# Kernel optimization log

Measured on AMD Instinct MI355X. Metric: run time of the kernel, lower is better.

Reference implementation:

```python
import jax, jax.numpy as jnp
import numpy as np

B, QUE, VAL, D = 4, 128, 128, 512

def setup_inputs() -> dict:
    key = jax.random.key(0)
    k = jax.random.split(key, 8)
    return {
        "qs_1": jax.random.normal(k[0], (B, QUE, D), jnp.float32),
        "qs_2": jax.random.normal(k[1], (B, QUE, D), jnp.float32),  # unused by forward, kept for signature fidelity
        "ks":   jax.random.normal(k[2], (B, VAL, D), jnp.float32),
        "vs":   jax.random.normal(k[3], (B, VAL, D), jnp.float32),
        "sg_mask": jax.random.randint(k[4], (B, VAL), 0, 2).astype(bool),  # True = masked
        "W1":  jax.random.normal(k[5], (D, D), jnp.float32) / np.sqrt(D),
        "b1":  jnp.zeros((D,), jnp.float32),
        "Wse": jax.random.normal(k[6], (D, D), jnp.float32) / np.sqrt(D),
        "bse": jnp.zeros((D,), jnp.float32),
        "W2":  jax.random.normal(k[7], (D, 1), jnp.float32) / np.sqrt(D),
        "b2":  jnp.zeros((1,), jnp.float32),
    }

def reference(qs_1, qs_2, ks, vs, sg_mask, W1, b1, Wse, bse, W2, b2):
    # Pairwise query-key elementwise product: [B, que, val, d]
    x = qs_1[:, :, None, :] * ks[:, None, :, :]
    # linear1: Linear(d,d) + ReLU (dropout = identity at eval)
    h = jax.nn.relu(jnp.einsum('bqvd,de->bqve', x, W1) + b1)
    # linear2: Linear(d,1) + ReLU -> scalar score per (q, v) pair
    s = jax.nn.relu(jnp.einsum('bqvd,do->bqvo', h, W2) + b2)[..., 0]  # [B, que, val]
    m = sg_mask[:, None, :]                      # [B, 1, val], True = masked out
    # masked mean of h over the val axis (masked_fill(0) then divide by valid count)
    h = jnp.where(m[..., None], 0.0, h)
    denom = jnp.sum(~sg_mask, axis=-1).astype(h.dtype)      # [B]
    mean = h.sum(axis=2) / denom[:, None, None]             # [B, que, d]
    # squeeze-excitation gate: sigmoid(relu(Linear(d,d)))
    gate = jax.nn.sigmoid(jax.nn.relu(mean @ Wse + bse))    # [B, que, d]
    # masked softmax over val, weighted sum of values
    s = jnp.where(m, -1e9, s)
    w = jax.nn.softmax(s, axis=-1)                          # [B, que, val]
    out = jnp.einsum('bqv,bvd->bqd', w, vs)                 # [B, que, d]
    return gate * out
```

## Files before the change

### kernel.cpp

```cpp
#include <hip/hip_runtime.h>
#include <stdint.h>
#include <stddef.h>

#define BDIM 4
#define QUE  128
#define VAL  128
#define DD   512
#define BQ   (BDIM*QUE)
#define BK   64

typedef float    f32x4 __attribute__((ext_vector_type(4)));
typedef float    f32x2 __attribute__((ext_vector_type(2)));
typedef _Float16 f16x8 __attribute__((ext_vector_type(8)));
typedef _Float16 f16x4 __attribute__((ext_vector_type(4)));
typedef _Float16 f16x2 __attribute__((ext_vector_type(2)));

typedef const __attribute__((address_space(1))) void* gas_ptr;
typedef __attribute__((address_space(3))) void*       las_ptr;

__device__ __forceinline__ void async_copy16(const void* g, void* l) {
    __builtin_amdgcn_global_load_lds((gas_ptr)g, (las_ptr)l, 16, 0, 0);
}

__global__ __launch_bounds__(256) void prep_kernel(const float* __restrict__ W1,
                                                   _Float16* __restrict__ W1T,
                                                   const float* __restrict__ Wse,
                                                   _Float16* __restrict__ WseT,
                                                   const float* __restrict__ vs,
                                                   _Float16* __restrict__ vsT) {
    __shared__ float tile[32][33];
    const int tx = threadIdx.x & 31;
    const int ty = threadIdx.x >> 5;
    const int gx = blockIdx.x, gy = blockIdx.y;
    if (gy < 32) {
        const float* src = (gy < 16) ? W1  : Wse;
        _Float16*    dst = (gy < 16) ? W1T : WseT;
        int a0 = gx * 32;
        int b0 = (gy & 15) * 32;
        #pragma unroll
        for (int r = 0; r < 4; ++r)
            tile[ty + r*8][tx] = src[(size_t)(a0 + ty + r*8) * DD + b0 + tx];
        __syncthreads();
        #pragma unroll
        for (int r = 0; r < 4; ++r) {
            int el = ty + r*8;
            dst[(size_t)(b0 + el) * DD + a0 + tx] = (_Float16)tile[tx][el];
        }
    } else {
        int bb = gy - 32;
        const float* src = vs  + (size_t)bb * VAL * DD;
        _Float16*    dst = vsT + (size_t)bb * DD * VAL;
        int b0 = gx * 32;
        for (int vt = 0; vt < 4; ++vt) {
            int a0 = vt * 32;
            __syncthreads();
            #pragma unroll
            for (int r = 0; r < 4; ++r)
                tile[ty + r*8][tx] = src[(size_t)(a0 + ty + r*8) * DD + b0 + tx];
            __syncthreads();
            #pragma unroll
            for (int r = 0; r < 4; ++r) {
                int el = ty + r*8;
                dst[(size_t)(b0 + el) * VAL + a0 + tx] = (_Float16)tile[tx][el];
            }
        }
    }
}

__global__ __launch_bounds__(512, 4) void gemm_h_kernel(
    const float* __restrict__ qs1,
    const float* __restrict__ ks,
    const int*   __restrict__ sgmask,
    const _Float16* __restrict__ W1T,
    const float* __restrict__ b1,
    const float* __restrict__ W2,
    float* __restrict__ s_part,
    float* __restrict__ meansum)
{
    __shared__ _Float16 Ah[128 * BK];
    __shared__ _Float16 Bh[256 * BK];
    __shared__ float qrow[DD];
    __shared__ float sred[4][VAL];
    __shared__ float msumLDS[2][256];

    const int tid  = threadIdx.x;
    const int bq   = blockIdx.x;
    const int gy   = blockIdx.y;
    const int b    = bq >> 7;
    const int lane = tid & 63;
    const int wid  = tid >> 6;
    const int wm   = wid >> 2;
    const int wn   = wid & 3;
    const int quad = lane >> 4;
    const int lr   = lane & 15;

    if (tid < 128)
        *(f32x4*)(qrow + tid * 4) = *(const f32x4*)(qs1 + (size_t)bq * DD + tid * 4);

    f32x4 acc[4][4];
    #pragma unroll
    for (int i = 0; i < 4; ++i)
        #pragma unroll
        for (int j = 0; j < 4; ++j) acc[i][j] = (f32x4){0.f, 0.f, 0.f, 0.f};

    const int ar0 = tid >> 3;
    const int ar1 = 64 + ar0;
    const int slt = tid & 7;
    const int ca0 = (slt - (ar0 & 7)) & 7;
    const int ca1 = (slt - (ar1 & 7)) & 7;
    const float* ksrow0 = ks + ((size_t)b * VAL + ar0) * DD + ca0 * 8;
    const float* ksrow1 = ks + ((size_t)b * VAL + ar1) * DD + ca1 * 8;
    const float* qb0 = qrow + ca0 * 8;
    const float* qb1 = qrow + ca1 * 8;
    const int aoff0 = tid * 8;
    const int aoff1 = (512 + tid) * 8;

    const _Float16* gB[4];
    int ldsBoff[4];
    #pragma unroll
    for (int j = 0; j < 4; ++j) {
        int chunk = j * 512 + tid;
        int row   = chunk >> 3;
        int c     = ((chunk & 7) - (row & 7)) & 7;
        gB[j] = W1T + (size_t)(gy * 256 + row) * DD + c * 8;
        ldsBoff[j] = (j * 512 + wid * 64) * 8;
    }

    int faoff[4], fboff[4];
    #pragma unroll
    for (int mt = 0; mt < 4; ++mt) {
        int row = wm * 64 + mt * 16 + lr;
        faoff[mt] = row * BK + (((quad + row) & 7) << 3);
    }
    #pragma unroll
    for (int nt = 0; nt < 4; ++nt) {
        int row = wn * 64 + nt * 16 + lr;
        fboff[nt] = row * BK + (((quad + row) & 7) << 3);
    }
    __syncthreads();

    for (int kk = 0; kk < DD; kk += BK) {
        #pragma unroll
        for (int j = 0; j < 4; ++j)
            async_copy16(gB[j] + kk, &Bh[ldsBoff[j]]);
        {
            f32x4 kv0 = *(const f32x4*)(ksrow0 + kk);
            f32x4 kv1 = *(const f32x4*)(ksrow0 + kk + 4);
            f32x4 qv0 = *(const f32x4*)(qb0 + kk);
            f32x4 qv1 = *(const f32x4*)(qb0 + kk + 4);
            f16x8 av;
            #pragma unroll
            for (int c = 0; c < 4; ++c) {
                av[c]     = (_Float16)(kv0[c] * qv0[c]);
                av[c + 4] = (_Float16)(kv1[c] * qv1[c]);
            }
            *(f16x8*)&Ah[aoff0] = av;
        }
        {
            f32x4 kv0 = *(const f32x4*)(ksrow1 + kk);
            f32x4 kv1 = *(const f32x4*)(ksrow1 + kk + 4);
            f32x4 qv0 = *(const f32x4*)(qb1 + kk);
            f32x4 qv1 = *(const f32x4*)(qb1 + kk + 4);
            f16x8 av;
            #pragma unroll
            for (int c = 0; c < 4; ++c) {
                av[c]     = (_Float16)(kv0[c] * qv0[c]);
                av[c + 4] = (_Float16)(kv1[c] * qv1[c]);
            }
            *(f16x8*)&Ah[aoff1] = av;
        }
        __syncthreads();

        #pragma unroll
        for (int sub = 0; sub < 2; ++sub) {
            const int sx = sub << 5;
            f16x8 fa[4];
            #pragma unroll
            for (int mt = 0; mt < 4; ++mt)
                fa[mt] = *(const f16x8*)&Ah[faoff[mt] ^ sx];
            #pragma unroll
            for (int nt = 0; nt < 4; ++nt) {
                f16x8 fb = *(const f16x8*)&Bh[fboff[nt] ^ sx];
                #pragma unroll
                for (int mt = 0; mt < 4; ++mt)
                    acc[mt][nt] = __builtin_amdgcn_mfma_f32_16x16x32_f16(fa[mt], fb, acc[mt][nt], 0, 0, 0);
            }
        }
        __syncthreads();
    }

    float b1v[4], w2v[4];
    #pragma unroll
    for (int nt = 0; nt < 4; ++nt) {
        int col = gy*256 + wn*64 + nt*16 + lr;
        b1v[nt] = b1[col];
        w2v[nt] = W2[col];
    }
    float msum[4] = {0.f, 0.f, 0.f, 0.f};
    #pragma unroll
    for (int mt = 0; mt < 4; ++mt) {
        #pragma unroll
        for (int reg = 0; reg < 4; ++reg) {
            int v = wm*64 + mt*16 + quad*4 + reg;
            int masked = sgmask[b * VAL + v];
            float sacc = 0.f;
            #pragma unroll
            for (int nt = 0; nt < 4; ++nt) {
                float h = acc[mt][nt][reg] + b1v[nt];
                h = fmaxf(h, 0.f);
                sacc += h * w2v[nt];
                if (!masked) msum[nt] += h;
            }
            sacc += __shfl_xor(sacc, 1);
            sacc += __shfl_xor(sacc, 2);
            sacc += __shfl_xor(sacc, 4);
            sacc += __shfl_xor(sacc, 8);
            if (lr == 0) sred[wn][v] = sacc;
        }
    }
    #pragma unroll
    for (int nt = 0; nt < 4; ++nt) {
        float m = msum[nt];
        m += __shfl_xor(m, 16);
        m += __shfl_xor(m, 32);
        if (lane < 16) msumLDS[wm][wn*64 + nt*16 + lr] = m;
    }
    __syncthreads();
    if (tid < 128) {
        s_part[((size_t)bq * 2 + gy) * VAL + tid] =
            sred[0][tid] + sred[1][tid] + sred[2][tid] + sred[3][tid];
    } else if (tid >= 256) {
        int c = tid - 256;
        meansum[(size_t)bq * DD + gy*256 + c] = msumLDS[0][c] + msumLDS[1][c];
    }
}

__global__ __launch_bounds__(64) void mid_kernel(
    const float* __restrict__ s_part,
    const float* __restrict__ meansum,
    const int*   __restrict__ sgmask,
    const float* __restrict__ b2,
    _Float16* __restrict__ wH,
    _Float16* __restrict__ meanH)
{
    const int bq = blockIdx.x;
    const int b  = bq >> 7;
    const int lane = threadIdx.x;
    const float* sp = s_part + (size_t)bq * 2 * VAL;
    float s0 = fmaxf(sp[lane]      + sp[128 + lane]      + b2[0], 0.f);
    float s1 = fmaxf(sp[64 + lane] + sp[192 + lane]      + b2[0], 0.f);
    int m0 = sgmask[b * VAL + lane], m1 = sgmask[b * VAL + 64 + lane];
    float cnt = (m0 ? 0.f : 1.f) + (m1 ? 0.f : 1.f);
    if (m0) s0 = -1e9f;
    if (m1) s1 = -1e9f;
    float mx = fmaxf(s0, s1);
    #pragma unroll
    for (int off = 32; off; off >>= 1) mx = fmaxf(mx, __shfl_xor(mx, off));
    float e0 = __expf(s0 - mx), e1 = __expf(s1 - mx);
    float se = e0 + e1;
    #pragma unroll
    for (int off = 32; off; off >>= 1) {
        se  += __shfl_xor(se, off);
        cnt += __shfl_xor(cnt, off);
    }
    float invse = 1.f / se;
    float invd  = 1.f / cnt;
    wH[(size_t)bq * VAL + lane]      = (_Float16)(e0 * invse);
    wH[(size_t)bq * VAL + 64 + lane] = (_Float16)(e1 * invse);
    f32x4 mA = *(const f32x4*)(meansum + (size_t)bq * DD + lane * 8);
    f32x4 mB = *(const f32x4*)(meansum + (size_t)bq * DD + lane * 8 + 4);
    f16x8 mh;
    #pragma unroll
    for (int c = 0; c < 4; ++c) {
        mh[c]     = (_Float16)(mA[c] * invd);
        mh[c + 4] = (_Float16)(mB[c] * invd);
    }
    *(f16x8*)(meanH + (size_t)bq * DD + lane * 8) = mh;
}

__global__ __launch_bounds__(64) void final_kernel(
    const _Float16* __restrict__ meanH,
    const _Float16* __restrict__ WseT,
    const _Float16* __restrict__ wH,
    const _Float16* __restrict__ vsT,
    const float* __restrict__ bse,
    float* __restrict__ out)
{
    const int lane = threadIdx.x;
    const int lr   = lane & 15;
    const int quad = lane >> 4;
    const int q0   = blockIdx.x * 32;
    const int d0   = blockIdx.y * 64;
    const int b    = q0 >> 7;

    f32x4 ga[2][4], oa[2][4];
    #pragma unroll
    for (int i = 0; i < 2; ++i)
        #pragma unroll
        for (int j = 0; j < 4; ++j) { ga[i][j] = (f32x4){0,0,0,0}; oa[i][j] = (f32x4){0,0,0,0}; }

    const _Float16* ap0 = meanH + (size_t)(q0 + lr) * DD + quad * 8;
    const _Float16* bp0 = WseT  + (size_t)(d0 + lr) * DD + quad * 8;
    #pragma unroll 2
    for (int kk = 0; kk < DD; kk += 32) {
        f16x8 am[2];
        #pragma unroll
        for (int mt = 0; mt < 2; ++mt)
            am[mt] = *(const f16x8*)(ap0 + (size_t)mt * 16 * DD + kk);
        #pragma unroll
        for (int nt = 0; nt < 4; ++nt) {
            f16x8 bw = *(const f16x8*)(bp0 + (size_t)nt * 16 * DD + kk);
            #pragma unroll
            for (int mt = 0; mt < 2; ++mt)
                ga[mt][nt] = __builtin_amdgcn_mfma_f32_16x16x32_f16(am[mt], bw, ga[mt][nt], 0, 0, 0);
        }
    }
    const _Float16* wp0 = wH  + (size_t)(q0 + lr) * VAL + quad * 8;
    const _Float16* vp0 = vsT + (size_t)b * DD * VAL + (size_t)(d0 + lr) * VAL + quad * 8;
    #pragma unroll
    for (int kk = 0; kk < VAL; kk += 32) {
        f16x8 am[2];
        #pragma unroll
        for (int mt = 0; mt < 2; ++mt)
            am[mt] = *(const f16x8*)(wp0 + (size_t)mt * 16 * VAL + kk);
        #pragma unroll
        for (int nt = 0; nt < 4; ++nt) {
            f16x8 bv = *(const f16x8*)(vp0 + (size_t)nt * 16 * VAL + kk);
            #pragma unroll
            for (int mt = 0; mt < 2; ++mt)
                oa[mt][nt] = __builtin_amdgcn_mfma_f32_16x16x32_f16(am[mt], bv, oa[mt][nt], 0, 0, 0);
        }
    }
    #pragma unroll
    for (int nt = 0; nt < 4; ++nt) {
        int col = d0 + nt * 16 + lr;
        float bsev = bse[col];
        #pragma unroll
        for (int mt = 0; mt < 2; ++mt) {
            #pragma unroll
            for (int reg = 0; reg < 4; ++reg) {
                int row = q0 + mt * 16 + quad * 4 + reg;
                float garg = ga[mt][nt][reg] + bsev;
                garg = fmaxf(garg, 0.f);
                float gate = 1.f / (1.f + __expf(-garg));
                out[(size_t)row * DD + col] = gate * oa[mt][nt][reg];
            }
        }
    }
}

extern "C" void kernel_launch(void* const* d_in, const int* in_sizes, int n_in,
                              void* d_out, int out_size, void* d_ws, size_t ws_size,
                              hipStream_t stream) {
    (void)in_sizes; (void)n_in; (void)out_size; (void)ws_size;
    const float* qs1 = (const float*)d_in[0];
    const float* ks  = (const float*)d_in[2];
    const float* vs  = (const float*)d_in[3];
    const int*   sg  = (const int*)d_in[4];
    const float* W1  = (const float*)d_in[5];
    const float* b1  = (const float*)d_in[6];
    const float* Wse = (const float*)d_in[7];
    const float* bse = (const float*)d_in[8];
    const float* W2  = (const float*)d_in[9];
    const float* b2  = (const float*)d_in[10];
    float* out = (float*)d_out;

    char* ws = (char*)d_ws;
    _Float16* W1T    = (_Float16*)(ws);
    _Float16* WseT   = (_Float16*)(ws + (512 << 10));
    _Float16* vsT    = (_Float16*)(ws + (1 << 20));
    float*    s_part = (float*)(ws + (1536 << 10));
    float*    msum   = (float*)(ws + (2 << 20));
    _Float16* wH     = (_Float16*)(ws + (3 << 20));
    _Float16* meanH  = (_Float16*)(ws + (3 << 20) + (128 << 10));

    prep_kernel<<<dim3(16, 36), 256, 0, stream>>>(W1, W1T, Wse, WseT, vs, vsT);
    gemm_h_kernel<<<dim3(BQ, 2), 512, 0, stream>>>(qs1, ks, sg, W1T, b1, W2, s_part, msum);
    mid_kernel<<<BQ, 64, 0, stream>>>(s_part, msum, sg, b2, wH, meanH);
    final_kernel<<<dim3(16, 8), 64, 0, stream>>>(meanH, WseT, wH, vsT, bse, out);
}
```

Before: 134.0 us.

## Fuse softmax/mean normalization into final gate GEMM kernel with LDS tiling

Removes the separate mid_kernel by computing the masked softmax weights and normalized mean inside the final kernel, staging them in LDS as fp16. The final kernel is retiled to 32x32 output tiles with 4 waves per block and 256 blocks, loading Wse and vs tiles through LDS. This drops one launch and the global round trip of wH/meanH, but each block now recomputes softmax and mean conversion for its 32 rows across 16 column blocks, which adds redundant work.

```diff
diff --git a/kernel.cpp b/kernel.cpp
--- a/kernel.cpp
+++ b/kernel.cpp
@@ -235,117 +235,141 @@
     }
 }
 
-__global__ __launch_bounds__(64) void mid_kernel(
+#define MPAD 514
+#define WPAD 130
+__global__ __launch_bounds__(256) void final_kernel(
     const float* __restrict__ s_part,
-    const float* __restrict__ meansum,
+    const float* __restrict__ msum,
     const int*   __restrict__ sgmask,
-    const float* __restrict__ b2,
-    _Float16* __restrict__ wH,
-    _Float16* __restrict__ meanH)
-{
-    const int bq = blockIdx.x;
-    const int b  = bq >> 7;
-    const int lane = threadIdx.x;
-    const float* sp = s_part + (size_t)bq * 2 * VAL;
-    float s0 = fmaxf(sp[lane]      + sp[128 + lane]      + b2[0], 0.f);
-    float s1 = fmaxf(sp[64 + lane] + sp[192 + lane]      + b2[0], 0.f);
-    int m0 = sgmask[b * VAL + lane], m1 = sgmask[b * VAL + 64 + lane];
-    float cnt = (m0 ? 0.f : 1.f) + (m1 ? 0.f : 1.f);
-    if (m0) s0 = -1e9f;
-    if (m1) s1 = -1e9f;
-    float mx = fmaxf(s0, s1);
-    #pragma unroll
-    for (int off = 32; off; off >>= 1) mx = fmaxf(mx, __shfl_xor(mx, off));
-    float e0 = __expf(s0 - mx), e1 = __expf(s1 - mx);
-    float se = e0 + e1;
-    #pragma unroll
-    for (int off = 32; off; off >>= 1) {
-        se  += __shfl_xor(se, off);
-        cnt += __shfl_xor(cnt, off);
-    }
-    float invse = 1.f / se;
-    float invd  = 1.f / cnt;
-    wH[(size_t)bq * VAL + lane]      = (_Float16)(e0 * invse);
-    wH[(size_t)bq * VAL + 64 + lane] = (_Float16)(e1 * invse);
-    f32x4 mA = *(const f32x4*)(meansum + (size_t)bq * DD + lane * 8);
-    f32x4 mB = *(const f32x4*)(meansum + (size_t)bq * DD + lane * 8 + 4);
-    f16x8 mh;
-    #pragma unroll
-    for (int c = 0; c < 4; ++c) {
-        mh[c]     = (_Float16)(mA[c] * invd);
-        mh[c + 4] = (_Float16)(mB[c] * invd);
-    }
-    *(f16x8*)(meanH + (size_t)bq * DD + lane * 8) = mh;
-}
-
-__global__ __launch_bounds__(64) void final_kernel(
-    const _Float16* __restrict__ meanH,
     const _Float16* __restrict__ WseT,
-    const _Float16* __restrict__ wH,
     const _Float16* __restrict__ vsT,
     const float* __restrict__ bse,
+    const float* __restrict__ b2,
     float* __restrict__ out)
 {
-    const int lane = threadIdx.x;
+    __shared__ _Float16 meanLDS[32 * MPAD];
+    __shared__ _Float16 wLDS[32 * WPAD];
+    __shared__ _Float16 BLDS[32 * WPAD];
+
+    const int tid  = threadIdx.x;
+    const int q0   = blockIdx.x * 32;
+    const int d0   = blockIdx.y * 32;
+    const int b    = q0 >> 7;
+    const int lane = tid & 63;
+    const int wid  = tid >> 6;
+    const int wm   = wid >> 1, wn = wid & 1;
+    const int quad = lane >> 4;
     const int lr   = lane & 15;
-    const int quad = lane >> 4;
-    const int q0   = blockIdx.x * 32;
-    const int d0   = blockIdx.y * 64;
-    const int b    = q0 >> 7;
-
-    f32x4 ga[2][4], oa[2][4];
-    #pragma unroll
-    for (int i = 0; i < 2; ++i)
-        #pragma unroll
-        for (int j = 0; j < 4; ++j) { ga[i][j] = (f32x4){0,0,0,0}; oa[i][j] = (f32x4){0,0,0,0}; }
-
-    const _Float16* ap0 = meanH + (size_t)(q0 + lr) * DD + quad * 8;
-    const _Float16* bp0 = WseT  + (size_t)(d0 + lr) * DD + quad * 8;
-    #pragma unroll 2
-    for (int kk = 0; kk < DD; kk += 32) {
-        f16x8 am[2];
-        #pragma unroll
-        for (int mt = 0; mt < 2; ++mt)
-            am[mt] = *(const f16x8*)(ap0 + (size_t)mt * 16 * DD + kk);
-        #pragma unroll
-        for (int nt = 0; nt < 4; ++nt) {
-            f16x8 bw = *(const f16x8*)(bp0 + (size_t)nt * 16 * DD + kk);
-            #pragma unroll
-            for (int mt = 0; mt < 2; ++mt)
-                ga[mt][nt] = __builtin_amdgcn_mfma_f32_16x16x32_f16(am[mt], bw, ga[mt][nt], 0, 0, 0);
-        }
-    }
-    const _Float16* wp0 = wH  + (size_t)(q0 + lr) * VAL + quad * 8;
-    const _Float16* vp0 = vsT + (size_t)b * DD * VAL + (size_t)(d0 + lr) * VAL + quad * 8;
-    #pragma unroll
-    for (int kk = 0; kk < VAL; kk += 32) {
-        f16x8 am[2];
-        #pragma unroll
-        for (int mt = 0; mt < 2; ++mt)
-            am[mt] = *(const f16x8*)(wp0 + (size_t)mt * 16 * VAL + kk);
-        #pragma unroll
-        for (int nt = 0; nt < 4; ++nt) {
-            f16x8 bv = *(const f16x8*)(vp0 + (size_t)nt * 16 * VAL + kk);
-            #pragma unroll
-            for (int mt = 0; mt < 2; ++mt)
-                oa[mt][nt] = __builtin_amdgcn_mfma_f32_16x16x32_f16(am[mt], bv, oa[mt][nt], 0, 0, 0);
-        }
-    }
-    #pragma unroll
-    for (int nt = 0; nt < 4; ++nt) {
-        int col = d0 + nt * 16 + lr;
-        float bsev = bse[col];
-        #pragma unroll
-        for (int mt = 0; mt < 2; ++mt) {
-            #pragma unroll
-            for (int reg = 0; reg < 4; ++reg) {
-                int row = q0 + mt * 16 + quad * 4 + reg;
-                float garg = ga[mt][nt][reg] + bsev;
-                garg = fmaxf(garg, 0.f);
-                float gate = 1.f / (1.f + __expf(-garg));
-                out[(size_t)row * DD + col] = gate * oa[mt][nt][reg];
-            }
-        }
+    const int r    = tid >> 3;
+    const int sl   = tid & 7;
+
+    const float b2v = b2[0];
+    const int   bq  = q0 + r;
+    const float* sp = s_part + (size_t)bq * 2 * VAL;
+    float vals[16];
+    int   msk[16];
+    float smax = -3.4e38f;
+    #pragma unroll
+    for (int i4 = 0; i4 < 4; ++i4) {
+        f32x4 s0 = *(const f32x4*)(sp + sl*16 + i4*4);
+        f32x4 s1 = *(const f32x4*)(sp + VAL + sl*16 + i4*4);
+        #pragma unroll
+        for (int j = 0; j < 4; ++j) {
+            int idx = i4*4 + j;
+            int v   = sl*16 + idx;
+            float s = fmaxf(s0[j] + s1[j] + b2v, 0.f);
+            int m   = sgmask[b * VAL + v];
+            msk[idx] = m;
+            if (m) s = -1e9f;
+            vals[idx] = s;
+            smax = fmaxf(smax, s);
+        }
+    }
+    smax = fmaxf(smax, __shfl_xor(smax, 1));
+    smax = fmaxf(smax, __shfl_xor(smax, 2));
+    smax = fmaxf(smax, __shfl_xor(smax, 4));
+    float sume = 0.f, cnt = 0.f;
+    #pragma unroll
+    for (int i = 0; i < 16; ++i) {
+        vals[i] = __expf(vals[i] - smax);
+        sume += vals[i];
+        cnt  += msk[i] ? 0.f : 1.f;
+    }
+    sume += __shfl_xor(sume, 1);  cnt += __shfl_xor(cnt, 1);
+    sume += __shfl_xor(sume, 2);  cnt += __shfl_xor(cnt, 2);
+    sume += __shfl_xor(sume, 4);  cnt += __shfl_xor(cnt, 4);
+    const float invse = 1.f / sume;
+    const float invd  = 1.f / cnt;
+    f16x8 wv0, wv1;
+    #pragma unroll
+    for (int i = 0; i < 8; ++i) {
+        wv0[i] = (_Float16)(vals[i]     * invse);
+        wv1[i] = (_Float16)(vals[i + 8] * invse);
+    }
+    *(f16x8*)&wLDS[r * WPAD + sl*16]     = wv0;
+    *(f16x8*)&wLDS[r * WPAD + sl*16 + 8] = wv1;
+    const float* mrow = msum + (size_t)bq * DD;
+    #pragma unroll
+    for (int i = 0; i < 8; ++i) {
+        int e = i*64 + sl*8;
+        f32x4 m0 = *(const f32x4*)(mrow + e);
+        f32x4 m1 = *(const f32x4*)(mrow + e + 4);
+        f16x8 mh;
+        #pragma unroll
+        for (int c = 0; c < 4; ++c) {
+            mh[c]     = (_Float16)(m0[c] * invd);
+            mh[c + 4] = (_Float16)(m1[c] * invd);
+        }
+        *(f16x8*)&meanLDS[r * MPAD + e] = mh;
+    }
+    __syncthreads();
+
+    f32x4 accg = (f32x4){0.f, 0.f, 0.f, 0.f};
+    const int a_off = (wm*16 + lr) * MPAD + quad*8;
+    const int b_off = (wn*16 + lr) * WPAD + quad*8;
+    const int st_off = r * WPAD + sl*16;
+    #pragma unroll
+    for (int cc = 0; cc < 4; ++cc) {
+        const _Float16* wrow = WseT + (size_t)(d0 + r) * DD + cc*128 + sl*16;
+        f16x8 bw0 = *(const f16x8*)(wrow);
+        f16x8 bw1 = *(const f16x8*)(wrow + 8);
+        *(f16x8*)&BLDS[st_off]     = bw0;
+        *(f16x8*)&BLDS[st_off + 8] = bw1;
+        __syncthreads();
+        #pragma unroll
+        for (int ks = 0; ks < 4; ++ks) {
+            f16x8 fa = *(const f16x8*)&meanLDS[a_off + cc*128 + ks*32];
+            f16x8 fb = *(const f16x8*)&BLDS[b_off + ks*32];
+            accg = __builtin_amdgcn_mfma_f32_16x16x32_f16(fa, fb, accg, 0, 0, 0);
+        }
+        __syncthreads();
+    }
+
+    {
+        const _Float16* vrow = vsT + ((size_t)b * DD + d0 + r) * VAL + sl*16;
+        f16x8 bv0 = *(const f16x8*)(vrow);
+        f16x8 bv1 = *(const f16x8*)(vrow + 8);
+        *(f16x8*)&BLDS[st_off]     = bv0;
+        *(f16x8*)&BLDS[st_off + 8] = bv1;
+    }
+    __syncthreads();
+    f32x4 acco = (f32x4){0.f, 0.f, 0.f, 0.f};
+    const int w_off = (wm*16 + lr) * WPAD + quad*8;
+    #pragma unroll
+    for (int ks = 0; ks < 4; ++ks) {
+        f16x8 fa = *(const f16x8*)&wLDS[w_off + ks*32];
+        f16x8 fb = *(const f16x8*)&BLDS[b_off + ks*32];
+        acco = __builtin_amdgcn_mfma_f32_16x16x32_f16(fa, fb, acco, 0, 0, 0);
+    }
+
+    const int d = d0 + wn*16 + lr;
+    const float bsev = bse[d];
+    #pragma unroll
+    for (int reg = 0; reg < 4; ++reg) {
+        int q = q0 + wm*16 + quad*4 + reg;
+        float g = fmaxf(accg[reg] + bsev, 0.f);
+        g = 1.f / (1.f + __expf(-g));
+        out[(size_t)q * DD + d] = g * acco[reg];
     }
 }
 
@@ -371,11 +395,8 @@
     _Float16* vsT    = (_Float16*)(ws + (1 << 20));
     float*    s_part = (float*)(ws + (1536 << 10));
     float*    msum   = (float*)(ws + (2 << 20));
-    _Float16* wH     = (_Float16*)(ws + (3 << 20));
-    _Float16* meanH  = (_Float16*)(ws + (3 << 20) + (128 << 10));
 
     prep_kernel<<<dim3(16, 36), 256, 0, stream>>>(W1, W1T, Wse, WseT, vs, vsT);
     gemm_h_kernel<<<dim3(BQ, 2), 512, 0, stream>>>(qs1, ks, sg, W1T, b1, W2, s_part, msum);
-    mid_kernel<<<BQ, 64, 0, stream>>>(s_part, msum, sg, b2, wH, meanH);
-    final_kernel<<<dim3(16, 8), 64, 0, stream>>>(meanH, WseT, wH, vsT, bse, out);
+    final_kernel<<<dim3(16, 16), 256, 0, stream>>>(s_part, msum, sg, WseT, vsT, bse, b2, out);
 }
```

After: 131.9 us. No clear change (-1.5%).
